# Kernel optimization log

Hardware: AMD Instinct MI355X
Metric: run time of the kernel (lower is better)

## Reference

```python
import jax, jax.numpy as jnp
import numpy as np

D_MODEL = 1024
NUM_HEADS = 16


def setup_inputs() -> dict:
    key = jax.random.key(0)
    ks = jax.random.split(key, 5)
    B, S, D = 2, 2048, D_MODEL
    x = jax.random.normal(ks[0], (B, S, D), dtype=jnp.float32)
    # nn.Linear(d_model, d_model, bias=False) weights, shape [out, in]
    scale = 1.0 / np.sqrt(D)
    Wq = jax.random.normal(ks[1], (D, D), dtype=jnp.float32) * scale
    Wk = jax.random.normal(ks[2], (D, D), dtype=jnp.float32) * scale
    Wv = jax.random.normal(ks[3], (D, D), dtype=jnp.float32) * scale
    Wo = jax.random.normal(ks[4], (D, D), dtype=jnp.float32) * scale
    return {"x": x, "Wq": Wq, "Wk": Wk, "Wv": Wv, "Wo": Wo}


def reference(x, Wq, Wk, Wv, Wo):
    B, S, D = x.shape
    H = NUM_HEADS
    dh = D // H
    # projections: x @ W.T (Linear without bias)
    q = (x @ Wq.T).reshape(B, S, H, dh).transpose(0, 2, 1, 3)  # [B,H,S,dh]
    k = (x @ Wk.T).reshape(B, S, H, dh).transpose(0, 2, 1, 3)
    v = (x @ Wv.T).reshape(B, S, H, dh).transpose(0, 2, 1, 3)
    scores = jnp.einsum("bhqd,bhkd->bhqk", q, k) / jnp.sqrt(jnp.float32(dh))
    # causal mask: positions j > i get -inf before softmax
    causal = jnp.triu(jnp.ones((S, S), dtype=bool), k=1)
    scores = jnp.where(causal, -jnp.inf, scores)
    attn = jax.nn.softmax(scores, axis=-1)  # [B,H,S,S]
    out = jnp.einsum("bhqk,bhkd->bhqd", attn, v)  # [B,H,S,dh]
    out = out.transpose(0, 2, 1, 3).reshape(B, S, D)
    return out @ Wo.T
```

## Files before the change

### kernel.cpp

```cpp
#include <hip/hip_runtime.h>

typedef __attribute__((ext_vector_type(8))) __bf16 bf16x8;
typedef __attribute__((ext_vector_type(4))) __bf16 bf16x4;
typedef __attribute__((ext_vector_type(4))) float f32x4;

static constexpr int S = 2048;
static constexpr int D = 1024;
static constexpr int BATCH = 2;
static constexpr int M_ROWS = BATCH * S;

#define GLOAD_LDS16(gp, lp)                                                        \
  __builtin_amdgcn_global_load_lds((const __attribute__((address_space(1))) void*)(gp), \
                                   (__attribute__((address_space(3))) void*)(lp), 16, 0, 0)

__global__ __launch_bounds__(256) void cast_f32_bf16(const float* __restrict__ in,
                                                     __bf16* __restrict__ out) {
  int i = (blockIdx.x * 256 + threadIdx.x) * 4;
  *reinterpret_cast<bf16x4*>(out + i) =
      __builtin_convertvector(*reinterpret_cast<const f32x4*>(in + i), bf16x4);
}

__global__ __launch_bounds__(256) void cast_w4(const float* __restrict__ w0, const float* __restrict__ w1,
                                               const float* __restrict__ w2, const float* __restrict__ w3,
                                               __bf16* __restrict__ o0, __bf16* __restrict__ o1,
                                               __bf16* __restrict__ o2, __bf16* __restrict__ o3) {
  const float* in = blockIdx.y == 0 ? w0 : blockIdx.y == 1 ? w1 : blockIdx.y == 2 ? w2 : w3;
  __bf16* out = blockIdx.y == 0 ? o0 : blockIdx.y == 1 ? o1 : blockIdx.y == 2 ? o2 : o3;
  int i = (blockIdx.x * 256 + threadIdx.x) * 4;
  *reinterpret_cast<bf16x4*>(out + i) =
      __builtin_convertvector(*reinterpret_cast<const f32x4*>(in + i), bf16x4);
}

template <typename OutT>
__device__ __forceinline__ void gemm_core(const __bf16* __restrict__ A,
                                          const __bf16* __restrict__ Bm,
                                          OutT* __restrict__ C, int m0, int n0, int K, int ldc,
                                          __bf16* At, __bf16* Bt) {
  const int tid = threadIdx.x;
  const int w = tid >> 6, l = tid & 63;
  const int wr = w >> 1, wc = w & 1;
  const int ln = l & 15, gr = l >> 4;

  const int srow = w * 32 + (l >> 2);
  const int scol = (l & 3) * 8;
  const size_t aoff = (size_t)(m0 + srow) * K + scol;
  const size_t boff = (size_t)(n0 + srow) * K + scol;
  __bf16* lA = At + w * 2 * 512;
  __bf16* lB = Bt + w * 2 * 512;

  f32x4 acc[4][4] = {};

  for (int k0 = 0; k0 < K; k0 += 32) {
    __syncthreads();
    GLOAD_LDS16(A + aoff + k0, lA);
    GLOAD_LDS16(A + aoff + (size_t)16 * K + k0, lA + 512);
    GLOAD_LDS16(Bm + boff + k0, lB);
    GLOAD_LDS16(Bm + boff + (size_t)16 * K + k0, lB + 512);
    __syncthreads();

    bf16x8 af[4], bfr[4];
#pragma unroll
    for (int mi = 0; mi < 4; mi++)
      af[mi] = *reinterpret_cast<const bf16x8*>(&At[(wr * 64 + mi * 16 + ln) * 32 + gr * 8]);
#pragma unroll
    for (int ni = 0; ni < 4; ni++)
      bfr[ni] = *reinterpret_cast<const bf16x8*>(&Bt[(wc * 64 + ni * 16 + ln) * 32 + gr * 8]);
#pragma unroll
    for (int mi = 0; mi < 4; mi++)
#pragma unroll
      for (int ni = 0; ni < 4; ni++)
        acc[mi][ni] = __builtin_amdgcn_mfma_f32_16x16x32_bf16(af[mi], bfr[ni], acc[mi][ni], 0, 0, 0);
  }

#pragma unroll
  for (int mi = 0; mi < 4; mi++)
#pragma unroll
    for (int ni = 0; ni < 4; ni++)
#pragma unroll
      for (int r = 0; r < 4; r++) {
        int row = m0 + wr * 64 + mi * 16 + gr * 4 + r;
        int col = n0 + wc * 64 + ni * 16 + ln;
        float v = acc[mi][ni][r];
        if constexpr (__is_same(OutT, float))
          C[(size_t)row * ldc + col] = v;
        else
          C[(size_t)row * ldc + col] = (__bf16)v;
      }
}

__global__ __launch_bounds__(256) void qkv_gemm(const __bf16* __restrict__ xb,
                                                const __bf16* __restrict__ wq,
                                                const __bf16* __restrict__ wk,
                                                const __bf16* __restrict__ wv,
                                                __bf16* __restrict__ q, __bf16* __restrict__ k,
                                                __bf16* __restrict__ vt) {
  __shared__ __bf16 At[128 * 32];
  __shared__ __bf16 Bt[128 * 32];
  const int id = blockIdx.x;
  const __bf16 *A, *B;
  __bf16* C;
  int m0, n0, ldc;
  if (id < 512) {
    A = xb;
    B = (id < 256) ? wq : wk;
    C = (id < 256) ? q : k;
    int t = id & 255;
    m0 = (t >> 3) * 128;
    n0 = (t & 7) * 128;
    ldc = 1024;
  } else {
    int t = id - 512;
    A = wv;
    B = xb;
    C = vt;
    m0 = (t & 7) * 128;
    n0 = (t >> 3) * 128;
    ldc = 4096;
  }
  gemm_core<__bf16>(A, B, C, m0, n0, 1024, ldc, At, Bt);
}

__global__ __launch_bounds__(256) void wo_gemm(const __bf16* __restrict__ ob,
                                               const __bf16* __restrict__ wo,
                                               float* __restrict__ out) {
  __shared__ __bf16 At[128 * 32];
  __shared__ __bf16 Bt[128 * 32];
  gemm_core<float>(ob, wo, out, blockIdx.y * 128, blockIdx.x * 128, 1024, 1024, At, Bt);
}

__global__ __launch_bounds__(512) void attn_kernel(const __bf16* __restrict__ Qb,
                                                   const __bf16* __restrict__ Kb,
                                                   const __bf16* __restrict__ VTb,
                                                   __bf16* __restrict__ Ob) {
  __shared__ __bf16 pt_all[8][32][40];

  const int lin = blockIdx.x;
  const int wid = ((lin & 7) << 5) | (lin >> 3);
  const int bh = wid >> 3;
  const int j = wid & 7;
  const int b = bh >> 4, h = bh & 15;

  const int tid = threadIdx.x;
  const int w = tid >> 6, l = tid & 63;
  const int ln = l & 15, gr = l >> 4;

  int qt;
  switch (w) {
    case 0: qt = j; break;
    case 1: qt = 16 + j; break;
    case 2: qt = 15 - j; break;
    case 3: qt = 31 - j; break;
    case 4: qt = 63 - j; break;
    case 5: qt = 47 - j; break;
    case 6: qt = 48 + j; break;
    default: qt = 32 + j; break;
  }
  const int q0 = qt * 32;
  const int n = qt + 1;

  const __bf16* Qp = Qb + (size_t)b * S * D + h * 64;
  const __bf16* Kp = Kb + (size_t)b * S * D + h * 64;
  const __bf16* Vt = VTb + (size_t)(h * 64) * M_ROWS + b * S;
  __bf16 (*pt)[40] = pt_all[w];

  const float SCALE2 = 0.125f * 1.44269504f;
  const float NEG = -1e30f;

  bf16x8 qf[2][2];
#pragma unroll
  for (int m = 0; m < 2; m++)
#pragma unroll
    for (int s = 0; s < 2; s++)
      qf[m][s] = *reinterpret_cast<const bf16x8*>(
          Qp + (size_t)(q0 + m * 16 + ln) * D + s * 32 + gr * 8);

  f32x4 oacc[2][4] = {};
  float mr[2] = {NEG, NEG}, ls[2] = {0.f, 0.f};

  auto loadK = [&](bf16x8 (&dst)[2][2], int kk) {
#pragma unroll
    for (int c = 0; c < 2; c++)
#pragma unroll
      for (int s = 0; s < 2; s++)
        dst[c][s] = *reinterpret_cast<const bf16x8*>(
            Kp + (size_t)(kk + c * 16 + ln) * D + s * 32 + gr * 8);
  };
  auto loadV = [&](bf16x8 (&dst)[4], int kk) {
#pragma unroll
    for (int t = 0; t < 4; t++)
      dst[t] = *reinterpret_cast<const bf16x8*>(
          Vt + (size_t)(t * 16 + ln) * M_ROWS + kk + gr * 8);
  };
  auto qk = [&](f32x4 (&st)[2][2], bf16x8 (&kf)[2][2]) {
    __builtin_amdgcn_s_setprio(1);
#pragma unroll
    for (int c = 0; c < 2; c++)
#pragma unroll
      for (int m = 0; m < 2; m++) {
        f32x4 z = {};
        z = __builtin_amdgcn_mfma_f32_16x16x32_bf16(kf[c][0], qf[m][0], z, 0, 0, 0);
        z = __builtin_amdgcn_mfma_f32_16x16x32_bf16(kf[c][1], qf[m][1], z, 0, 0, 0);
        st[c][m] = z;
      }
    __builtin_amdgcn_s_setprio(0);
  };
  auto smpv = [&](f32x4 (&st)[2][2], bf16x8 (&vf)[4], int t) {
    const bool tail = (t == n - 1);
#pragma unroll
    for (int m = 0; m < 2; m++) {
      float pv[8];
      float tm = NEG;
#pragma unroll
      for (int c = 0; c < 2; c++)
#pragma unroll
        for (int r = 0; r < 4; r++) {
          float v = st[c][m][r] * SCALE2;
          if (tail) v = (c * 16 + 4 * gr + r <= m * 16 + ln) ? v : NEG;
          pv[c * 4 + r] = v;
          tm = fmaxf(tm, v);
        }
      tm = fmaxf(tm, __shfl_xor(tm, 16));
      tm = fmaxf(tm, __shfl_xor(tm, 32));
      if (!__all(tm - mr[m] <= 8.0f)) {
        float nm = fmaxf(mr[m], tm);
        float a = __builtin_exp2f(mr[m] - nm);
        mr[m] = nm;
        ls[m] *= a;
#pragma unroll
        for (int tt = 0; tt < 4; tt++)
#pragma unroll
          for (int r = 0; r < 4; r++) oacc[m][tt][r] *= a;
      }
      float ps = 0.f;
#pragma unroll
      for (int i = 0; i < 8; i++) {
        pv[i] = __builtin_exp2f(pv[i] - mr[m]);
        ps += pv[i];
      }
      ps += __shfl_xor(ps, 16);
      ps += __shfl_xor(ps, 32);
      ls[m] += ps;
#pragma unroll
      for (int c = 0; c < 2; c++) {
        bf16x4 pk = {(__bf16)pv[c * 4 + 0], (__bf16)pv[c * 4 + 1],
                     (__bf16)pv[c * 4 + 2], (__bf16)pv[c * 4 + 3]};
        *reinterpret_cast<bf16x4*>(&pt[m * 16 + ln][c * 16 + 4 * gr]) = pk;
      }
    }
    __builtin_amdgcn_s_setprio(1);
#pragma unroll
    for (int m = 0; m < 2; m++) {
      bf16x8 pp = *reinterpret_cast<const bf16x8*>(&pt[m * 16 + ln][gr * 8]);
#pragma unroll
      for (int tt = 0; tt < 4; tt++)
        oacc[m][tt] = __builtin_amdgcn_mfma_f32_16x16x32_bf16(vf[tt], pp, oacc[m][tt], 0, 0, 0);
    }
    __builtin_amdgcn_s_setprio(0);
  };

  f32x4 stA[2][2], stB[2][2];
  bf16x8 kf0[2][2], kf1[2][2], vf0[4], vf1[4];

  loadK(kf0, 0);
  loadV(vf0, 0);
  if (n > 1) {
    loadK(kf1, 32);
    loadV(vf1, 32);
  }
  qk(stA, kf0);

  auto iter_step = [&](f32x4 (&stCur)[2][2], f32x4 (&stNxt)[2][2],
                       bf16x8 (&kfNxt)[2][2], bf16x8 (&kfTgt)[2][2],
                       bf16x8 (&vfCur)[4], int t) {
    if (t + 1 < n) qk(stNxt, kfNxt);
    if (t + 2 < n) loadK(kfTgt, 32 * (t + 2));
    smpv(stCur, vfCur, t);
    if (t + 2 < n) loadV(vfCur, 32 * (t + 2));
  };

  int t = 0;
  for (;;) {
    iter_step(stA, stB, kf1, kf0, vf0, t);
    if (++t >= n) break;
    iter_step(stB, stA, kf0, kf1, vf1, t);
    if (++t >= n) break;
  }

#pragma unroll
  for (int m = 0; m < 2; m++) {
    float inv = 1.0f / ls[m];
    size_t row = (size_t)(b * S + q0 + m * 16 + ln);
#pragma unroll
    for (int tt = 0; tt < 4; tt++) {
      bf16x4 ov = {(__bf16)(oacc[m][tt][0] * inv), (__bf16)(oacc[m][tt][1] * inv),
                   (__bf16)(oacc[m][tt][2] * inv), (__bf16)(oacc[m][tt][3] * inv)};
      *reinterpret_cast<bf16x4*>(Ob + row * D + h * 64 + tt * 16 + gr * 4) = ov;
    }
  }
}

extern "C" void kernel_launch(void* const* d_in, const int* in_sizes, int n_in,
                              void* d_out, int out_size, void* d_ws, size_t ws_size,
                              hipStream_t stream) {
  const float* x = (const float*)d_in[0];
  const float* Wq = (const float*)d_in[1];
  const float* Wk = (const float*)d_in[2];
  const float* Wv = (const float*)d_in[3];
  const float* Wo = (const float*)d_in[4];
  float* out = (float*)d_out;

  char* ws = (char*)d_ws;
  const size_t MB = 1024 * 1024;
  __bf16* xb = (__bf16*)(ws + 0 * MB);
  __bf16* qb = (__bf16*)(ws + 8 * MB);
  __bf16* kb = (__bf16*)(ws + 16 * MB);
  __bf16* vtb = (__bf16*)(ws + 24 * MB);
  __bf16* ob = (__bf16*)(ws + 32 * MB);
  __bf16* wqb = (__bf16*)(ws + 40 * MB);
  __bf16* wkb = (__bf16*)(ws + 42 * MB);
  __bf16* wvb = (__bf16*)(ws + 44 * MB);
  __bf16* wob = (__bf16*)(ws + 46 * MB);

  const int nx = M_ROWS * D;
  const int nw = D * D;

  cast_f32_bf16<<<nx / 4 / 256, 256, 0, stream>>>(x, xb);
  cast_w4<<<dim3(nw / 4 / 256, 4), 256, 0, stream>>>(Wq, Wk, Wv, Wo, wqb, wkb, wvb, wob);

  qkv_gemm<<<768, 256, 0, stream>>>(xb, wqb, wkb, wvb, qb, kb, vtb);

  attn_kernel<<<256, 512, 0, stream>>>(qb, kb, vtb, ob);

  wo_gemm<<<dim3(8, 32), 256, 0, stream>>>(ob, wob, out);
}
```

Measured before the change: 149.6 us.

## Switch attention to 32x32x16 MFMA with register-shuffled P, dropping LDS staging

Rewrites the attention inner loop so each wave uses 32x32x16 bf16 MFMAs instead of 16x16x32. The QK^T accumulator layout now lets the probability tile be rebuilt in registers through lane xor-32 shuffles, so the per-wave LDS buffer and its writes and reads go away. Row max and sum need fewer cross-lane shuffles, the scale is folded into one fma before exp2, and launch bounds ask for two blocks per CU. The cost is larger per-lane accumulators, which raises register pressure and may conflict with the occupancy hint.

Result: no change. 147.7 us (-1.3%).

```diff
diff --git a/kernel.cpp b/kernel.cpp
--- a/kernel.cpp
+++ b/kernel.cpp
@@ -2,7 +2,10 @@
 
 typedef __attribute__((ext_vector_type(8))) __bf16 bf16x8;
 typedef __attribute__((ext_vector_type(4))) __bf16 bf16x4;
+typedef __attribute__((ext_vector_type(2))) __bf16 bf16x2;
 typedef __attribute__((ext_vector_type(4))) float f32x4;
+typedef __attribute__((ext_vector_type(16))) float f32x16;
+typedef __attribute__((ext_vector_type(4))) unsigned uint4v;
 
 static constexpr int S = 2048;
 static constexpr int D = 1024;
@@ -128,12 +131,10 @@
   gemm_core<float>(ob, wo, out, blockIdx.y * 128, blockIdx.x * 128, 1024, 1024, At, Bt);
 }
 
-__global__ __launch_bounds__(512) void attn_kernel(const __bf16* __restrict__ Qb,
-                                                   const __bf16* __restrict__ Kb,
-                                                   const __bf16* __restrict__ VTb,
-                                                   __bf16* __restrict__ Ob) {
-  __shared__ __bf16 pt_all[8][32][40];
-
+__global__ __launch_bounds__(512, 2) void attn_kernel(const __bf16* __restrict__ Qb,
+                                                      const __bf16* __restrict__ Kb,
+                                                      const __bf16* __restrict__ VTb,
+                                                      __bf16* __restrict__ Ob) {
   const int lin = blockIdx.x;
   const int wid = ((lin & 7) << 5) | (lin >> 3);
   const int bh = wid >> 3;
@@ -142,7 +143,7 @@
 
   const int tid = threadIdx.x;
   const int w = tid >> 6, l = tid & 63;
-  const int ln = l & 15, gr = l >> 4;
+  const int q31 = l & 31, hi = l >> 5;
 
   int qt;
   switch (w) {
@@ -161,105 +162,120 @@
   const __bf16* Qp = Qb + (size_t)b * S * D + h * 64;
   const __bf16* Kp = Kb + (size_t)b * S * D + h * 64;
   const __bf16* Vt = VTb + (size_t)(h * 64) * M_ROWS + b * S;
-  __bf16 (*pt)[40] = pt_all[w];
 
   const float SCALE2 = 0.125f * 1.44269504f;
   const float NEG = -1e30f;
-
-  bf16x8 qf[2][2];
-#pragma unroll
-  for (int m = 0; m < 2; m++)
-#pragma unroll
-    for (int s = 0; s < 2; s++)
-      qf[m][s] = *reinterpret_cast<const bf16x8*>(
-          Qp + (size_t)(q0 + m * 16 + ln) * D + s * 32 + gr * 8);
-
-  f32x4 oacc[2][4] = {};
-  float mr[2] = {NEG, NEG}, ls[2] = {0.f, 0.f};
-
-  auto loadK = [&](bf16x8 (&dst)[2][2], int kk) {
-#pragma unroll
-    for (int c = 0; c < 2; c++)
-#pragma unroll
-      for (int s = 0; s < 2; s++)
-        dst[c][s] = *reinterpret_cast<const bf16x8*>(
-            Kp + (size_t)(kk + c * 16 + ln) * D + s * 32 + gr * 8);
-  };
-  auto loadV = [&](bf16x8 (&dst)[4], int kk) {
-#pragma unroll
-    for (int t = 0; t < 4; t++)
-      dst[t] = *reinterpret_cast<const bf16x8*>(
-          Vt + (size_t)(t * 16 + ln) * M_ROWS + kk + gr * 8);
-  };
-  auto qk = [&](f32x4 (&st)[2][2], bf16x8 (&kf)[2][2]) {
+  const float THR_RAW = 8.0f / SCALE2;
+
+  bf16x8 qf[4];
+#pragma unroll
+  for (int ds = 0; ds < 4; ds++)
+    qf[ds] = *reinterpret_cast<const bf16x8*>(
+        Qp + (size_t)(q0 + q31) * D + ds * 16 + hi * 8);
+
+  f32x16 oacc[2] = {};
+  float mr = NEG, ls = 0.f;
+
+  auto loadK = [&](bf16x8 (&dst)[4], int kk) {
+#pragma unroll
+    for (int ds = 0; ds < 4; ds++)
+      dst[ds] = *reinterpret_cast<const bf16x8*>(
+          Kp + (size_t)(kk + q31) * D + ds * 16 + hi * 8);
+  };
+  auto loadV = [&](bf16x8 (&dst)[2][2], int kk) {
+#pragma unroll
+    for (int d0 = 0; d0 < 2; d0++)
+#pragma unroll
+      for (int ks = 0; ks < 2; ks++)
+        dst[d0][ks] = *reinterpret_cast<const bf16x8*>(
+            Vt + (size_t)(d0 * 32 + q31) * M_ROWS + kk + ks * 16 + hi * 8);
+  };
+  auto qk = [&](f32x16& st, bf16x8 (&kf)[4]) {
+    f32x16 z = {};
     __builtin_amdgcn_s_setprio(1);
 #pragma unroll
-    for (int c = 0; c < 2; c++)
-#pragma unroll
-      for (int m = 0; m < 2; m++) {
-        f32x4 z = {};
-        z = __builtin_amdgcn_mfma_f32_16x16x32_bf16(kf[c][0], qf[m][0], z, 0, 0, 0);
-        z = __builtin_amdgcn_mfma_f32_16x16x32_bf16(kf[c][1], qf[m][1], z, 0, 0, 0);
-        st[c][m] = z;
+    for (int ds = 0; ds < 4; ds++)
+      z = __builtin_amdgcn_mfma_f32_32x32x16_bf16(kf[ds], qf[ds], z, 0, 0, 0);
+    __builtin_amdgcn_s_setprio(0);
+    st = z;
+  };
+
+  auto pack2 = [](float x, float y) -> unsigned {
+    bf16x2 p;
+    p[0] = (__bf16)x;
+    p[1] = (__bf16)y;
+    return __builtin_bit_cast(unsigned, p);
+  };
+
+  auto smpv = [&](f32x16& st, bf16x8 (&vf)[2][2], int t) {
+    const bool tail = (t == n - 1);
+    float pv[16];
+#pragma unroll
+    for (int r = 0; r < 16; r++) {
+      float v = st[r];
+      if (tail) {
+        int keyidx = (r & 3) + 8 * (r >> 2) + 4 * hi;
+        v = (keyidx <= q31) ? v : NEG;
       }
-    __builtin_amdgcn_s_setprio(0);
-  };
-  auto smpv = [&](f32x4 (&st)[2][2], bf16x8 (&vf)[4], int t) {
-    const bool tail = (t == n - 1);
-#pragma unroll
-    for (int m = 0; m < 2; m++) {
-      float pv[8];
-      float tm = NEG;
-#pragma unroll
-      for (int c = 0; c < 2; c++)
-#pragma unroll
-        for (int r = 0; r < 4; r++) {
-          float v = st[c][m][r] * SCALE2;
-          if (tail) v = (c * 16 + 4 * gr + r <= m * 16 + ln) ? v : NEG;
-          pv[c * 4 + r] = v;
-          tm = fmaxf(tm, v);
-        }
-      tm = fmaxf(tm, __shfl_xor(tm, 16));
-      tm = fmaxf(tm, __shfl_xor(tm, 32));
-      if (!__all(tm - mr[m] <= 8.0f)) {
-        float nm = fmaxf(mr[m], tm);
-        float a = __builtin_exp2f(mr[m] - nm);
-        mr[m] = nm;
-        ls[m] *= a;
-#pragma unroll
-        for (int tt = 0; tt < 4; tt++)
-#pragma unroll
-          for (int r = 0; r < 4; r++) oacc[m][tt][r] *= a;
-      }
-      float ps = 0.f;
-#pragma unroll
-      for (int i = 0; i < 8; i++) {
-        pv[i] = __builtin_exp2f(pv[i] - mr[m]);
-        ps += pv[i];
-      }
-      ps += __shfl_xor(ps, 16);
-      ps += __shfl_xor(ps, 32);
-      ls[m] += ps;
-#pragma unroll
-      for (int c = 0; c < 2; c++) {
-        bf16x4 pk = {(__bf16)pv[c * 4 + 0], (__bf16)pv[c * 4 + 1],
-                     (__bf16)pv[c * 4 + 2], (__bf16)pv[c * 4 + 3]};
-        *reinterpret_cast<bf16x4*>(&pt[m * 16 + ln][c * 16 + 4 * gr]) = pk;
-      }
+      pv[r] = v;
+    }
+    float t8[8], t4[4];
+#pragma unroll
+    for (int i = 0; i < 8; i++) t8[i] = fmaxf(pv[i], pv[i + 8]);
+#pragma unroll
+    for (int i = 0; i < 4; i++) t4[i] = fmaxf(t8[i], t8[i + 4]);
+    float tm = fmaxf(fmaxf(t4[0], t4[1]), fmaxf(t4[2], t4[3]));
+    tm = fmaxf(tm, __shfl_xor(tm, 32));
+    if (!__all(tm - mr <= THR_RAW)) {
+      float nm = fmaxf(mr, tm);
+      float a = __builtin_exp2f((mr - nm) * SCALE2);
+      mr = nm;
+      ls *= a;
+#pragma unroll
+      for (int d0 = 0; d0 < 2; d0++)
+#pragma unroll
+        for (int r = 0; r < 16; r++) oacc[d0][r] *= a;
+    }
+    const float mrs = mr * SCALE2;
+#pragma unroll
+    for (int r = 0; r < 16; r++)
+      pv[r] = __builtin_exp2f(__builtin_fmaf(pv[r], SCALE2, -mrs));
+    float s8[8], s4[4];
+#pragma unroll
+    for (int i = 0; i < 8; i++) s8[i] = pv[i] + pv[i + 8];
+#pragma unroll
+    for (int i = 0; i < 4; i++) s4[i] = s8[i] + s8[i + 4];
+    float ps = (s4[0] + s4[1]) + (s4[2] + s4[3]);
+    ps += __shfl_xor(ps, 32);
+    ls += ps;
+
+    unsigned dw[8];
+#pragma unroll
+    for (int bb = 0; bb < 4; bb++) {
+      dw[2 * bb] = pack2(pv[4 * bb], pv[4 * bb + 1]);
+      dw[2 * bb + 1] = pack2(pv[4 * bb + 2], pv[4 * bb + 3]);
     }
     __builtin_amdgcn_s_setprio(1);
 #pragma unroll
-    for (int m = 0; m < 2; m++) {
-      bf16x8 pp = *reinterpret_cast<const bf16x8*>(&pt[m * 16 + ln][gr * 8]);
-#pragma unroll
-      for (int tt = 0; tt < 4; tt++)
-        oacc[m][tt] = __builtin_amdgcn_mfma_f32_16x16x32_bf16(vf[tt], pp, oacc[m][tt], 0, 0, 0);
+    for (int ks = 0; ks < 2; ks++) {
+      unsigned s0 = hi ? dw[4 * ks + 0] : dw[4 * ks + 2];
+      unsigned s1 = hi ? dw[4 * ks + 1] : dw[4 * ks + 3];
+      unsigned r0 = (unsigned)__shfl_xor((int)s0, 32);
+      unsigned r1 = (unsigned)__shfl_xor((int)s1, 32);
+      uint4v uv;
+      uv.x = hi ? r0 : dw[4 * ks + 0];
+      uv.y = hi ? r1 : dw[4 * ks + 1];
+      uv.z = hi ? dw[4 * ks + 2] : r0;
+      uv.w = hi ? dw[4 * ks + 3] : r1;
+      bf16x8 pb = __builtin_bit_cast(bf16x8, uv);
+      oacc[0] = __builtin_amdgcn_mfma_f32_32x32x16_bf16(vf[0][ks], pb, oacc[0], 0, 0, 0);
+      oacc[1] = __builtin_amdgcn_mfma_f32_32x32x16_bf16(vf[1][ks], pb, oacc[1], 0, 0, 0);
     }
     __builtin_amdgcn_s_setprio(0);
   };
 
-  f32x4 stA[2][2], stB[2][2];
-  bf16x8 kf0[2][2], kf1[2][2], vf0[4], vf1[4];
+  f32x16 stA, stB;
+  bf16x8 kf0[4], kf1[4], vf0[2][2], vf1[2][2];
 
   loadK(kf0, 0);
   loadV(vf0, 0);
@@ -269,9 +285,8 @@
   }
   qk(stA, kf0);
 
-  auto iter_step = [&](f32x4 (&stCur)[2][2], f32x4 (&stNxt)[2][2],
-                       bf16x8 (&kfNxt)[2][2], bf16x8 (&kfTgt)[2][2],
-                       bf16x8 (&vfCur)[4], int t) {
+  auto iter_step = [&](f32x16& stCur, f32x16& stNxt, bf16x8 (&kfNxt)[4],
+                       bf16x8 (&kfTgt)[4], bf16x8 (&vfCur)[2][2], int t) {
     if (t + 1 < n) qk(stNxt, kfNxt);
     if (t + 2 < n) loadK(kfTgt, 32 * (t + 2));
     smpv(stCur, vfCur, t);
@@ -286,16 +301,17 @@
     if (++t >= n) break;
   }
 
-#pragma unroll
-  for (int m = 0; m < 2; m++) {
-    float inv = 1.0f / ls[m];
-    size_t row = (size_t)(b * S + q0 + m * 16 + ln);
-#pragma unroll
-    for (int tt = 0; tt < 4; tt++) {
-      bf16x4 ov = {(__bf16)(oacc[m][tt][0] * inv), (__bf16)(oacc[m][tt][1] * inv),
-                   (__bf16)(oacc[m][tt][2] * inv), (__bf16)(oacc[m][tt][3] * inv)};
-      *reinterpret_cast<bf16x4*>(Ob + row * D + h * 64 + tt * 16 + gr * 4) = ov;
-    }
+  {
+    float inv = 1.0f / ls;
+    size_t row = (size_t)(b * S + q0 + q31);
+#pragma unroll
+    for (int d0 = 0; d0 < 2; d0++)
+#pragma unroll
+      for (int bb = 0; bb < 4; bb++) {
+        bf16x4 ov = {(__bf16)(oacc[d0][4 * bb + 0] * inv), (__bf16)(oacc[d0][4 * bb + 1] * inv),
+                     (__bf16)(oacc[d0][4 * bb + 2] * inv), (__bf16)(oacc[d0][4 * bb + 3] * inv)};
+        *reinterpret_cast<bf16x4*>(Ob + row * D + h * 64 + d0 * 32 + 8 * bb + 4 * hi) = ov;
+      }
   }
 }
 
```
